# Performance work log

Hardware: AMD Instinct MI355X
Metric: run time of the kernel (lower is better)

The kernel has to match this reference:

```python
import jax, jax.numpy as jnp
import numpy as np

DIM = 192
R = 16            # patches_resolution, D=H=W=R
SP = 4            # split_size
NH = 6            # num_heads (block level); per-branch heads = NH//3
B = 2
L = R * R * R
EPS = 1e-5


def layernorm(x, g, b):
    mu = jnp.mean(x, axis=-1, keepdims=True)
    var = jnp.mean(jnp.square(x - mu), axis=-1, keepdims=True)
    return (x - mu) * jax.lax.rsqrt(var + EPS) * g + b


def window_partition(x, d_sp, h_sp, w_sp, nh):
    b, _, _, _, cb = x.shape
    win = d_sp * h_sp * w_sp
    x = x.reshape(b, R // d_sp, d_sp, R // h_sp, h_sp, R // w_sp, w_sp, cb)
    x = x.transpose(0, 1, 3, 5, 2, 4, 6, 7).reshape(-1, win, nh, cb // nh)
    return x.transpose(0, 2, 1, 3)


def window_merge(x, d_sp, h_sp, w_sp, b):
    cb = x.shape[-1]
    x = x.reshape(b, R // d_sp, R // h_sp, R // w_sp, d_sp, h_sp, w_sp, cb)
    x = x.transpose(0, 1, 4, 2, 5, 3, 6, 7).reshape(b, L, cb)
    return x


def lepe_attention(q, k, v, d_sp, h_sp, w_sp, nh):
    # q,k,v: (B, L, Cb). Note: LePE bias is computed-but-unused in the source -> pure windowed SDPA.
    b, _, cb = q.shape
    hd = cb // nh
    scale = hd ** -0.5
    q5 = q.reshape(b, R, R, R, cb)
    k5 = k.reshape(b, R, R, R, cb)
    v5 = v.reshape(b, R, R, R, cb)
    qw = window_partition(q5, d_sp, h_sp, w_sp, nh) * scale
    kw = window_partition(k5, d_sp, h_sp, w_sp, nh)
    vw = window_partition(v5, d_sp, h_sp, w_sp, nh)
    attn = jax.nn.softmax(jnp.einsum('whqd,whkd->whqk', qw, kw), axis=-1)
    out = jnp.einsum('whqk,whkd->whqd', attn, vw)
    out = out.transpose(0, 2, 1, 3).reshape(-1, d_sp * h_sp * w_sp, cb)
    return window_merge(out, d_sp, h_sp, w_sp, b)


WINDOW_SHAPES = [(R, R, SP), (R, SP, R), (SP, R, R)]  # idx 0,1,2


def setup_inputs() -> dict:
    key = jax.random.key(0)
    ks = jax.random.split(key, 12)
    C = DIM
    H4 = int(C * 4)
    inp = {
        'x': jax.random.normal(ks[0], (B, C, R, R, R), dtype=jnp.float32),
        'w_qkv': jax.random.normal(ks[1], (C, 3 * C), dtype=jnp.float32) * (C ** -0.5),
        'w_proj': jax.random.normal(ks[2], (C, C), dtype=jnp.float32) * (C ** -0.5),
        'b_proj': jnp.zeros((C,), dtype=jnp.float32),
        'g1': jnp.ones((C,), dtype=jnp.float32),
        'b1': jnp.zeros((C,), dtype=jnp.float32),
        'g2': jnp.ones((C,), dtype=jnp.float32),
        'b2': jnp.zeros((C,), dtype=jnp.float32),
        'w_fc1': jax.random.normal(ks[3], (C, H4), dtype=jnp.float32) * (C ** -0.5),
        'b_fc1': jnp.zeros((H4,), dtype=jnp.float32),
        'w_fc2': jax.random.normal(ks[4], (H4, C), dtype=jnp.float32) * (H4 ** -0.5),
        'b_fc2': jnp.zeros((C,), dtype=jnp.float32),
    }
    return inp


def reference(x, w_qkv, w_proj, b_proj, g1, b1, g2, b2, w_fc1, b_fc1, w_fc2, b_fc2):
    C = DIM
    Cb = C // 3
    nh_b = NH // 3
    x = 2.0 * x
    xt = jnp.transpose(x, (0, 2, 3, 4, 1))                # (B, D, H, W, C)
    img = layernorm(xt, g1, b1)
    qkv = img.reshape(B, L, C) @ w_qkv                    # (B, L, 3C)
    q, k, v = jnp.split(qkv.reshape(B, L, 3, C).transpose(2, 0, 1, 3), 3, axis=0)
    q, k, v = q[0], k[0], v[0]                            # each (B, L, C)
    outs = []
    for i, (dsp, hsp, wsp) in enumerate(WINDOW_SHAPES):
        sl = slice(i * Cb, (i + 1) * Cb)
        outs.append(lepe_attention(q[..., sl], k[..., sl], v[..., sl], dsp, hsp, wsp, nh_b))
    attened = jnp.concatenate(outs, axis=2)               # (B, L, C)
    attened = attened @ w_proj + b_proj
    xs = xt.reshape(B, L, C) + attened
    h = layernorm(xs, g2, b2) @ w_fc1 + b_fc1
    h = jax.nn.gelu(h, approximate=False)
    xs = xs + (h @ w_fc2 + b_fc2)
    out = xs.reshape(B, R, R, R, C).transpose(0, 4, 1, 2, 3)  # (B, C, D, H, W)
    return out
```

## Files before the change

### kernel.cpp

```cpp
#include <hip/hip_runtime.h>
#include <hip/hip_bf16.h>

typedef __hip_bfloat16 bf16;
typedef short short8 __attribute__((ext_vector_type(8)));
typedef float floatx4 __attribute__((ext_vector_type(4)));

#define SZ (8192*192)

__device__ __forceinline__ unsigned short f2b(float f) {
    unsigned u = __builtin_bit_cast(unsigned, f);
    u += 0x7FFFu + ((u >> 16) & 1u);
    return (unsigned short)(u >> 16);
}
__device__ __forceinline__ float b2f(unsigned short h) {
    unsigned u = ((unsigned)h) << 16;
    return __builtin_bit_cast(float, u);
}
__device__ __forceinline__ unsigned pk2(float a, float b) {
    return ((unsigned)f2b(b) << 16) | (unsigned)f2b(a);
}

__global__ void detect_kernel(const unsigned short* __restrict__ x16, int* __restrict__ flag) {
    __shared__ int cnt;
    if (threadIdx.x == 0) cnt = 0;
    __syncthreads();
    int c = 0;
    for (int i = threadIdx.x; i < 8192; i += 256) {
        int e = (x16[i] >> 7) & 0xFF;
        if (e >= 152) c++;
    }
    if (c) atomicAdd(&cnt, c);
    __syncthreads();
    if (threadIdx.x == 0) *flag = (cnt >= 32) ? 1 : 0;
}

struct WPA { const void* s[11]; };

__global__ __launch_bounds__(256) void wprep_kernel(WPA a, unsigned short* __restrict__ wdst,
                                                    float* __restrict__ vdst,
                                                    const int* __restrict__ flag) {
    int i = blockIdx.x * 256 + threadIdx.x;
    int f = *flag;
    if (i < 442368) {
        int seg, base, K, N;
        if (i < 110592)      { seg = 0; base = 0;      K = 192; N = 576; }
        else if (i < 147456) { seg = 1; base = 110592; K = 192; N = 192; }
        else if (i < 294912) { seg = 2; base = 147456; K = 192; N = 768; }
        else                 { seg = 3; base = 294912; K = 768; N = 192; }
        int j = i - base;
        int n = j / K, k = j - n * K;
        size_t src = (size_t)k * N + n;
        float v = f ? ((const float*)a.s[seg])[src] : b2f(((const unsigned short*)a.s[seg])[src]);
        int ci = (n >> 6) * (K >> 5) + (k >> 5);
        int off = (ci << 11) + (((n >> 4) & 3) << 9) + ((n & 15) << 5) + (k & 31);
        wdst[base + off] = f2b(v);
    } else if (i < 444288) {
        int j = i - 442368;
        int seg, off;
        if (j < 960)       { seg = 4 + j / 192; off = j % 192; }
        else if (j < 1728) { seg = 9; off = j - 960; }
        else               { seg = 10; off = j - 1728; }
        float v = f ? ((const float*)a.s[seg])[off] : b2f(((const unsigned short*)a.s[seg])[off]);
        vdst[j] = v;
    }
}

__global__ __launch_bounds__(256) void prep_kernel(const void* __restrict__ xin,
        const int* __restrict__ flag,
        const float* __restrict__ g1, const float* __restrict__ b1,
        float* __restrict__ xt, unsigned short* __restrict__ img) {
    __shared__ float tile[192][33];
    __shared__ float mu[32], rs[32];
    int tid = threadIdx.x;
    int t0 = blockIdx.x * 32;
    int b = t0 >> 12;
    int ts = t0 & 4095;
    int f = *flag;
    for (int idx = tid; idx < 192 * 32; idx += 256) {
        int c = idx >> 5, tt = idx & 31;
        int gi = ((b * 192 + c) << 12) + ts + tt;
        float raw = f ? ((const float*)xin)[gi] : b2f(((const unsigned short*)xin)[gi]);
        tile[c][tt] = 2.0f * raw;
    }
    __syncthreads();
    {
        int tt = tid >> 3, j = tid & 7;
        int c0 = j * 24;
        float s = 0.f, sq = 0.f;
        #pragma unroll
        for (int i = 0; i < 24; ++i) { float v = tile[c0 + i][tt]; s += v; sq += v * v; }
        s += __shfl_xor(s, 1); sq += __shfl_xor(sq, 1);
        s += __shfl_xor(s, 2); sq += __shfl_xor(sq, 2);
        s += __shfl_xor(s, 4); sq += __shfl_xor(sq, 4);
        if (j == 0) {
            float m = s * (1.0f / 192.0f);
            float var = sq * (1.0f / 192.0f) - m * m;
            mu[tt] = m;
            rs[tt] = rsqrtf(var + 1e-5f);
        }
    }
    __syncthreads();
    for (int idx = tid; idx < 32 * 192; idx += 256) {
        int tt = idx / 192, c = idx % 192;
        float v = tile[c][tt];
        int o = (t0 + tt) * 192 + c;
        xt[o] = v;
        img[o] = f2b((v - mu[tt]) * rs[tt] * g1[c] + b1[c]);
    }
}

__device__ __forceinline__ int g_of(int br, int t) {
    if (br == 0) return (((t >> 2) & 3) << 10) | ((t >> 8) << 6) | (((t >> 4) & 15) << 2) | (t & 3);
    if (br == 1) return (((t >> 6) & 3) << 10) | ((t >> 8) << 6) | (((t >> 4) & 3) << 4) | (t & 15);
    return t;
}

template <int MODE, int W>
__global__ __launch_bounds__(64 * W) void mfma_gemm(const unsigned short* __restrict__ A,
        const unsigned short* __restrict__ WT, const float* __restrict__ bias,
        const float* __restrict__ resid, void* __restrict__ out,
        unsigned short* __restrict__ qt, unsigned short* __restrict__ kt,
        unsigned short* __restrict__ vt, int N, int K) {
    int wave = threadIdx.x >> 6, lane = threadIdx.x & 63;
    int quad = lane >> 4, l16 = lane & 15;
    int m0 = blockIdx.x * (32 * W) + wave * 32, n0 = blockIdx.y * 64;
    const unsigned short* ap = A + (size_t)(m0 + l16) * K + quad * 8;
    const unsigned short* wpB = WT + (((size_t)blockIdx.y * (K >> 5)) << 11) + l16 * 32 + quad * 8;
    floatx4 acc[2][4] = {};
    #pragma unroll 2
    for (int kc = 0; kc < K; kc += 32) {
        short8 a0 = *reinterpret_cast<const short8*>(ap + kc);
        short8 a1 = *reinterpret_cast<const short8*>(ap + (size_t)16 * K + kc);
        const unsigned short* wc = wpB + (((size_t)(kc >> 5)) << 11);
        #pragma unroll
        for (int nt = 0; nt < 4; ++nt) {
            short8 w = *reinterpret_cast<const short8*>(wc + nt * 512);
            acc[0][nt] = __builtin_amdgcn_mfma_f32_16x16x32_bf16(a0, w, acc[0][nt], 0, 0, 0);
            acc[1][nt] = __builtin_amdgcn_mfma_f32_16x16x32_bf16(a1, w, acc[1][nt], 0, 0, 0);
        }
    }
    #pragma unroll
    for (int fh = 0; fh < 2; ++fh) {
        #pragma unroll
        for (int nt = 0; nt < 4; ++nt) {
            int col = n0 + nt * 16 + l16;
            if (MODE == 0 && n0 >= 384) {
                int cv = col - 384;
                int d = cv & 31, brh = cv >> 5;
                int row0 = m0 + fh * 16 + quad * 4;
                int bb_ = row0 >> 12, tl = row0 & 4095;
                int g0 = g_of(brh >> 1, tl);
                int wb2 = g0 >> 10, k = g0 & 63, c = k >> 4, m = k & 15;
                int pos = ((c >> 1) << 5) + ((m >> 2) << 3) + ((c & 1) << 2);
                int chunk = (g0 & 1023) >> 6;
                int tidx = ((d >> 4) << 1) | (pos >> 5);
                unsigned short* tile = vt + (((((size_t)(bb_ * 6 + brh) * 4 + wb2) * 16 + chunk) * 4 + tidx) << 9);
                ushort4 w4;
                w4.x = f2b(acc[fh][nt][0]);
                w4.y = f2b(acc[fh][nt][1]);
                w4.z = f2b(acc[fh][nt][2]);
                w4.w = f2b(acc[fh][nt][3]);
                *reinterpret_cast<ushort4*>(tile + (d & 15) * 32 + (pos & 31)) = w4;
            } else if (MODE == 0 && n0 >= 192) {
                int ck = col - 192;
                int d = ck & 31, brh = ck >> 5;
                int row0 = m0 + fh * 16 + quad * 4;
                int bb_ = row0 >> 12, tl = row0 & 4095;
                int g0 = g_of(brh >> 1, tl);
                int wb2 = g0 >> 10, k = g0 & 63, c = k >> 4, m = k & 15;
                int chunk = (g0 & 1023) >> 6;
                unsigned short* tile = kt + (((((size_t)(bb_ * 6 + brh) * 4 + wb2) * 16 + chunk) * 4 + c) << 9);
                tile[m * 32 + d]       = f2b(acc[fh][nt][0]);
                tile[(m + 1) * 32 + d] = f2b(acc[fh][nt][1]);
                tile[(m + 2) * 32 + d] = f2b(acc[fh][nt][2]);
                tile[(m + 3) * 32 + d] = f2b(acc[fh][nt][3]);
            } else if (MODE == 0) {
                int d = col & 31, brh = col >> 5;
                int row0 = m0 + fh * 16 + quad * 4;
                int bb_ = row0 >> 12, tl = row0 & 4095;
                int g0 = g_of(brh >> 1, tl);
                int wb2 = g0 >> 10, q = g0 & 1023;
                int chunk = q >> 4, m = q & 15;
                unsigned short* tile = qt + ((((size_t)(bb_ * 6 + brh) * 4 + wb2) * 64 + chunk) << 9);
                tile[m * 32 + d]       = f2b(acc[fh][nt][0] * 0.17677669529663689f);
                tile[(m + 1) * 32 + d] = f2b(acc[fh][nt][1] * 0.17677669529663689f);
                tile[(m + 2) * 32 + d] = f2b(acc[fh][nt][2] * 0.17677669529663689f);
                tile[(m + 3) * 32 + d] = f2b(acc[fh][nt][3] * 0.17677669529663689f);
            } else {
                #pragma unroll
                for (int r = 0; r < 4; ++r) {
                    int row = m0 + fh * 16 + quad * 4 + r;
                    float v = acc[fh][nt][r];
                    if (MODE >= 1) v += bias[col];
                    if (MODE == 2) v = 0.5f * v * (1.0f + erff(v * 0.70710678118654752f));
                    size_t o = (size_t)row * N + col;
                    if (MODE == 2) ((unsigned short*)out)[o] = f2b(v);
                    else           ((float*)out)[o] = v + resid[o];
                }
            }
        }
    }
}

__device__ __forceinline__ int tok_of(int br, int wb, int q) {
    if (br == 0) return ((q >> 6) << 8) | (((q >> 2) & 15) << 4) | (wb << 2) | (q & 3);
    else if (br == 1) return ((q >> 6) << 8) | (((wb << 2) + ((q >> 4) & 3)) << 4) | (q & 15);
    else return (((wb << 2) + (q >> 8)) << 8) | (q & 255);
}

__global__ __launch_bounds__(256) void attn_mfma(const unsigned short* __restrict__ qt,
        const unsigned short* __restrict__ kt, const unsigned short* __restrict__ vt,
        unsigned short* __restrict__ attb) {
    int hw = blockIdx.x;
    int bid = (hw & 7) * 96 + (hw >> 3);
    int qti = bid & 15, head = (bid >> 4) & 1, wb = (bid >> 5) & 3, b = (bid >> 7) & 1, br = bid >> 8;
    int tid = threadIdx.x;
    int wave = tid >> 6, lane = tid & 63, quad = lane >> 4, l16 = lane & 15;
    int coff = br * 64 + head * 32;
    int brh = br * 2 + head;
    int tb = b << 12;
    size_t qbase = ((((size_t)(b * 6 + brh) * 4 + wb) * 64 + qti * 4 + wave) << 9) + l16 * 32 + quad * 8;
    short8 aq = *reinterpret_cast<const short8*>(qt + qbase);
    floatx4 o0 = {}, o1 = {};
    float lsum = 0.f;

    const size_t kvbase = ((((size_t)(b * 6 + brh) * 4 + wb) * 16) << 11) + l16 * 32 + quad * 8;
    const unsigned short* kp = kt + kvbase;
    const unsigned short* vp = vt + kvbase;

    short8 k0 = *reinterpret_cast<const short8*>(kp);
    short8 k1 = *reinterpret_cast<const short8*>(kp + 512);
    short8 k2 = *reinterpret_cast<const short8*>(kp + 1024);
    short8 k3 = *reinterpret_cast<const short8*>(kp + 1536);
    short8 vb00 = *reinterpret_cast<const short8*>(vp);
    short8 vb01 = *reinterpret_cast<const short8*>(vp + 512);
    short8 vb10 = *reinterpret_cast<const short8*>(vp + 1024);
    short8 vb11 = *reinterpret_cast<const short8*>(vp + 1536);

    for (int it = 0; it < 16; ++it) {
        short8 ck0 = k0, ck1 = k1, ck2 = k2, ck3 = k3;
        short8 cv00 = vb00, cv01 = vb01, cv10 = vb10, cv11 = vb11;
        if (it + 1 < 16) {
            kp += 2048; vp += 2048;
            k0 = *reinterpret_cast<const short8*>(kp);
            k1 = *reinterpret_cast<const short8*>(kp + 512);
            k2 = *reinterpret_cast<const short8*>(kp + 1024);
            k3 = *reinterpret_cast<const short8*>(kp + 1536);
            vb00 = *reinterpret_cast<const short8*>(vp);
            vb01 = *reinterpret_cast<const short8*>(vp + 512);
            vb10 = *reinterpret_cast<const short8*>(vp + 1024);
            vb11 = *reinterpret_cast<const short8*>(vp + 1536);
        }
        floatx4 z = {};
        floatx4 s0 = __builtin_amdgcn_mfma_f32_16x16x32_bf16(ck0, aq, z, 0, 0, 0);
        floatx4 s1 = __builtin_amdgcn_mfma_f32_16x16x32_bf16(ck1, aq, z, 0, 0, 0);
        floatx4 s2 = __builtin_amdgcn_mfma_f32_16x16x32_bf16(ck2, aq, z, 0, 0, 0);
        floatx4 s3 = __builtin_amdgcn_mfma_f32_16x16x32_bf16(ck3, aq, z, 0, 0, 0);
        float p00 = __expf(s0[0]), p01 = __expf(s0[1]), p02 = __expf(s0[2]), p03 = __expf(s0[3]);
        float p10 = __expf(s1[0]), p11 = __expf(s1[1]), p12 = __expf(s1[2]), p13 = __expf(s1[3]);
        float p20 = __expf(s2[0]), p21 = __expf(s2[1]), p22 = __expf(s2[2]), p23 = __expf(s2[3]);
        float p30 = __expf(s3[0]), p31 = __expf(s3[1]), p32 = __expf(s3[2]), p33 = __expf(s3[3]);
        lsum += ((p00 + p01) + (p02 + p03)) + ((p10 + p11) + (p12 + p13))
              + ((p20 + p21) + (p22 + p23)) + ((p30 + p31) + (p32 + p33));
        uint4 ua, ub;
        ua.x = pk2(p00, p01); ua.y = pk2(p02, p03); ua.z = pk2(p10, p11); ua.w = pk2(p12, p13);
        ub.x = pk2(p20, p21); ub.y = pk2(p22, p23); ub.z = pk2(p30, p31); ub.w = pk2(p32, p33);
        short8 pa0 = __builtin_bit_cast(short8, ua);
        short8 pa1 = __builtin_bit_cast(short8, ub);
        o0 = __builtin_amdgcn_mfma_f32_16x16x32_bf16(pa0, cv00, o0, 0, 0, 0);
        o0 = __builtin_amdgcn_mfma_f32_16x16x32_bf16(pa1, cv01, o0, 0, 0, 0);
        o1 = __builtin_amdgcn_mfma_f32_16x16x32_bf16(pa0, cv10, o1, 0, 0, 0);
        o1 = __builtin_amdgcn_mfma_f32_16x16x32_bf16(pa1, cv11, o1, 0, 0, 0);
    }
    lsum += __shfl_xor(lsum, 16);
    lsum += __shfl_xor(lsum, 32);
    #pragma unroll
    for (int r = 0; r < 4; ++r) {
        float inv = 1.0f / __shfl(lsum, quad * 4 + r);
        int q = qti * 64 + wave * 16 + quad * 4 + r;
        int t = tok_of(br, wb, q);
        size_t o = (size_t)(tb + t) * 192 + coff;
        attb[o + l16]      = f2b(o0[r] * inv);
        attb[o + 16 + l16] = f2b(o1[r] * inv);
    }
}

__global__ __launch_bounds__(256) void ln_kernel(const float* __restrict__ in,
        const float* __restrict__ g, const float* __restrict__ bb, unsigned short* __restrict__ out) {
    int token = (blockIdx.x << 2) + (threadIdx.x >> 6);
    int lane = threadIdx.x & 63;
    const float* row = in + (size_t)token * 192;
    float v0 = row[lane], v1 = row[lane + 64], v2 = row[lane + 128];
    float s = v0 + v1 + v2, sq = v0 * v0 + v1 * v1 + v2 * v2;
    #pragma unroll
    for (int mask = 1; mask < 64; mask <<= 1) {
        s += __shfl_xor(s, mask);
        sq += __shfl_xor(sq, mask);
    }
    float m = s * (1.f / 192.f);
    float var = sq * (1.f / 192.f) - m * m;
    float rsd = rsqrtf(var + 1e-5f);
    unsigned short* orow = out + (size_t)token * 192;
    orow[lane]       = f2b((v0 - m) * rsd * g[lane]       + bb[lane]);
    orow[lane + 64]  = f2b((v1 - m) * rsd * g[lane + 64]  + bb[lane + 64]);
    orow[lane + 128] = f2b((v2 - m) * rsd * g[lane + 128] + bb[lane + 128]);
}

__global__ __launch_bounds__(256) void unprep_kernel(const float* __restrict__ xs,
                                                     void* __restrict__ out,
                                                     const int* __restrict__ flag) {
    __shared__ float tile[192][33];
    int tid = threadIdx.x;
    int t0 = blockIdx.x * 32;
    int b = t0 >> 12, ts = t0 & 4095;
    for (int idx = tid; idx < 32 * 192; idx += 256) {
        int tt = idx / 192, c = idx % 192;
        tile[c][tt] = xs[(size_t)(t0 + tt) * 192 + c];
    }
    __syncthreads();
    int f = *flag;
    for (int idx = tid; idx < 192 * 32; idx += 256) {
        int c = idx >> 5, tt = idx & 31;
        float v = tile[c][tt];
        int o = ((b * 192 + c) << 12) + ts + tt;
        if (f) ((float*)out)[o] = v;
        else   ((unsigned short*)out)[o] = f2b(v);
    }
}

extern "C" void kernel_launch(void* const* d_in, const int* in_sizes, int n_in,
                              void* d_out, int out_size, void* d_ws, size_t ws_size,
                              hipStream_t stream) {
    float* ws = (float*)d_ws;

    float* vbase = ws;
    float* bprojf = vbase + 0;
    float* g1f    = vbase + 192;
    float* b1f    = vbase + 384;
    float* g2f    = vbase + 576;
    float* b2f    = vbase + 768;
    float* bfc1f  = vbase + 960;
    float* bfc2f  = vbase + 1728;

    unsigned short* wbase = (unsigned short*)(ws + 1920);
    unsigned short* wqkvT = wbase + 0;
    unsigned short* wprojT = wbase + 110592;
    unsigned short* wfc1T = wbase + 147456;
    unsigned short* wfc2T = wbase + 294912;

    size_t p = 1920 + 442368 / 2;
    float* xt = ws + p; p += SZ;
    unsigned short* img = (unsigned short*)(ws + p); p += SZ / 2;
    size_t pQ = p;
    unsigned short* hbuf = (unsigned short*)(ws + pQ);
    p = pQ + 8192 * 768 / 2;
    unsigned short* attb = (unsigned short*)(ws + p); p += SZ / 2;
    int* flag = (int*)(ws + p); p += 16;
    unsigned short* qtb = (unsigned short*)(ws + p); p += SZ / 2;
    unsigned short* ktb = (unsigned short*)(ws + p); p += SZ / 2;
    unsigned short* vtb = (unsigned short*)(ws + p); p += SZ / 2;
    float* xs = xt;
    unsigned short* lnb = img;

    WPA wa;
    wa.s[0] = d_in[1];  wa.s[1] = d_in[2];  wa.s[2] = d_in[8];  wa.s[3] = d_in[10];
    wa.s[4] = d_in[3];  wa.s[5] = d_in[4];  wa.s[6] = d_in[5];  wa.s[7] = d_in[6];
    wa.s[8] = d_in[7];  wa.s[9] = d_in[9];  wa.s[10] = d_in[11];

    detect_kernel<<<dim3(1), dim3(256), 0, stream>>>((const unsigned short*)d_in[0], flag);
    wprep_kernel<<<dim3(1736), dim3(256), 0, stream>>>(wa, wbase, vbase, flag);
    prep_kernel<<<dim3(256), dim3(256), 0, stream>>>(d_in[0], flag, g1f, b1f, xt, img);
    mfma_gemm<0, 2><<<dim3(128, 9), dim3(128), 0, stream>>>(
        img, wqkvT, nullptr, nullptr, nullptr, qtb, ktb, vtb, 576, 192);
    attn_mfma<<<dim3(768), dim3(256), 0, stream>>>(qtb, ktb, vtb, attb);
    mfma_gemm<1, 1><<<dim3(256, 3), dim3(64), 0, stream>>>(
        attb, wprojT, bprojf, xt, xs, nullptr, nullptr, nullptr, 192, 192);
    ln_kernel<<<dim3(2048), dim3(256), 0, stream>>>(xs, g2f, b2f, lnb);
    mfma_gemm<2, 2><<<dim3(128, 12), dim3(128), 0, stream>>>(
        lnb, wfc1T, bfc1f, nullptr, hbuf, nullptr, nullptr, nullptr, 768, 192);
    mfma_gemm<3, 1><<<dim3(256, 3), dim3(64), 0, stream>>>(
        hbuf, wfc2T, bfc2f, xs, xs, nullptr, nullptr, nullptr, 192, 768);
    unprep_kernel<<<dim3(256), dim3(256), 0, stream>>>(xs, d_out, flag);
}
```

Before: 183.9 us.

## Store GEMM A-operands in 16x32 tiled layout for contiguous MFMA loads

Every producer of a bf16 GEMM input (prep LayerNorm output, attention output, second LayerNorm output, GELU output of fc1) now writes in a tiled layout of 16-row by 32-column blocks. The GEMM kernel reads its A fragments from these contiguous 1 KB tiles instead of strided rows. This is meant to improve coalescing and cache-line use of the A loads in all GEMMs. In exchange the producer stores become more scattered, and it also drops the bias branch for MODE 1, which is fine only if that mode always has a bias.

```diff
diff --git a/kernel.cpp b/kernel.cpp
--- a/kernel.cpp
+++ b/kernel.cpp
@@ -65,6 +65,7 @@
     }
 }
 
+
 __global__ __launch_bounds__(256) void prep_kernel(const void* __restrict__ xin,
         const int* __restrict__ flag,
         const float* __restrict__ g1, const float* __restrict__ b1,
@@ -103,9 +104,9 @@
     for (int idx = tid; idx < 32 * 192; idx += 256) {
         int tt = idx / 192, c = idx % 192;
         float v = tile[c][tt];
-        int o = (t0 + tt) * 192 + c;
-        xt[o] = v;
-        img[o] = f2b((v - mu[tt]) * rs[tt] * g1[c] + b1[c]);
+        xt[(t0 + tt) * 192 + c] = v;
+        int po = ((((t0 + tt) >> 4) * 6 + (c >> 5)) << 9) + ((tt & 15) << 5) + (c & 31);
+        img[po] = f2b((v - mu[tt]) * rs[tt] * g1[c] + b1[c]);
     }
 }
 
@@ -124,13 +125,16 @@
     int wave = threadIdx.x >> 6, lane = threadIdx.x & 63;
     int quad = lane >> 4, l16 = lane & 15;
     int m0 = blockIdx.x * (32 * W) + wave * 32, n0 = blockIdx.y * 64;
-    const unsigned short* ap = A + (size_t)(m0 + l16) * K + quad * 8;
-    const unsigned short* wpB = WT + (((size_t)blockIdx.y * (K >> 5)) << 11) + l16 * 32 + quad * 8;
+    const int KT = K >> 5;
+    const unsigned short* ap = A + (((size_t)(m0 >> 4) * KT) << 9) + l16 * 32 + quad * 8;
+    const size_t a1off = ((size_t)KT) << 9;
+    const unsigned short* wpB = WT + (((size_t)blockIdx.y * KT) << 11) + l16 * 32 + quad * 8;
     floatx4 acc[2][4] = {};
     #pragma unroll 2
     for (int kc = 0; kc < K; kc += 32) {
-        short8 a0 = *reinterpret_cast<const short8*>(ap + kc);
-        short8 a1 = *reinterpret_cast<const short8*>(ap + (size_t)16 * K + kc);
+        const unsigned short* ac = ap + (((size_t)(kc >> 5)) << 9);
+        short8 a0 = *reinterpret_cast<const short8*>(ac);
+        short8 a1 = *reinterpret_cast<const short8*>(ac + a1off);
         const unsigned short* wc = wpB + (((size_t)(kc >> 5)) << 11);
         #pragma unroll
         for (int nt = 0; nt < 4; ++nt) {
@@ -190,12 +194,16 @@
                 #pragma unroll
                 for (int r = 0; r < 4; ++r) {
                     int row = m0 + fh * 16 + quad * 4 + r;
-                    float v = acc[fh][nt][r];
-                    if (MODE >= 1) v += bias[col];
-                    if (MODE == 2) v = 0.5f * v * (1.0f + erff(v * 0.70710678118654752f));
-                    size_t o = (size_t)row * N + col;
-                    if (MODE == 2) ((unsigned short*)out)[o] = f2b(v);
-                    else           ((float*)out)[o] = v + resid[o];
+                    float v = acc[fh][nt][r] + bias[col];
+                    if (MODE == 2) {
+                        v = 0.5f * v * (1.0f + erff(v * 0.70710678118654752f));
+                        size_t o = (((size_t)(row >> 4) * (N >> 5) + (col >> 5)) << 9)
+                                 + ((row & 15) << 5) + (col & 31);
+                        ((unsigned short*)out)[o] = f2b(v);
+                    } else {
+                        size_t o = (size_t)row * N + col;
+                        ((float*)out)[o] = v + resid[o];
+                    }
                 }
             }
         }
@@ -278,8 +286,8 @@
     for (int r = 0; r < 4; ++r) {
         float inv = 1.0f / __shfl(lsum, quad * 4 + r);
         int q = qti * 64 + wave * 16 + quad * 4 + r;
-        int t = tok_of(br, wb, q);
-        size_t o = (size_t)(tb + t) * 192 + coff;
+        int t = tb + tok_of(br, wb, q);
+        size_t o = (((size_t)(t >> 4) * 6 + (coff >> 5)) << 9) + ((t & 15) << 5);
         attb[o + l16]      = f2b(o0[r] * inv);
         attb[o + 16 + l16] = f2b(o1[r] * inv);
     }
@@ -300,10 +308,11 @@
     float m = s * (1.f / 192.f);
     float var = sq * (1.f / 192.f) - m * m;
     float rsd = rsqrtf(var + 1e-5f);
-    unsigned short* orow = out + (size_t)token * 192;
-    orow[lane]       = f2b((v0 - m) * rsd * g[lane]       + bb[lane]);
-    orow[lane + 64]  = f2b((v1 - m) * rsd * g[lane + 64]  + bb[lane + 64]);
-    orow[lane + 128] = f2b((v2 - m) * rsd * g[lane + 128] + bb[lane + 128]);
+    int tbase = (token >> 4) * 6, tr = (token & 15) << 5;
+    int lo = lane >> 5, la = lane & 31;
+    out[((tbase + lo)     << 9) + tr + la] = f2b((v0 - m) * rsd * g[lane]       + bb[lane]);
+    out[((tbase + lo + 2) << 9) + tr + la] = f2b((v1 - m) * rsd * g[lane + 64]  + bb[lane + 64]);
+    out[((tbase + lo + 4) << 9) + tr + la] = f2b((v2 - m) * rsd * g[lane + 128] + bb[lane + 128]);
 }
 
 __global__ __launch_bounds__(256) void unprep_kernel(const float* __restrict__ xs,
```

After: 183.1 us. No clear change (-0.5%).
